# Performance work log

Measured on AMD Instinct MI355X. Metric: run time of the kernel, lower is better.

The kernel has to match this reference:

```python
import jax, jax.numpy as jnp
import numpy as np

# LightGCN propagation constants
N_USERS = 50000
N_ITEMS = 100000
N_NODES = N_USERS + N_ITEMS          # rows of the symmetric normalized adjacency
N_EDGES = 2400000                    # nnz of sparse adjacency (avg degree ~16)
LATENT_DIM = 64                      # config['latent_dim_rec']
N_LAYERS = 3                         # config['lightGCN_n_layers']
BATCH = 4096


def setup_inputs() -> dict:
    key = jax.random.key(0)
    ks = jax.random.split(key, 7)
    # Embedding tables, init std=0.1 as in nn.init.normal_(std=0.1)
    emb_user = 0.1 * jax.random.normal(ks[0], (N_USERS, LATENT_DIM), dtype=jnp.float32)
    emb_item = 0.1 * jax.random.normal(ks[1], (N_ITEMS, LATENT_DIM), dtype=jnp.float32)
    # Sparse normalized adjacency in COO form (fixed structure reused every layer)
    src = jax.random.randint(ks[2], (N_EDGES,), 0, N_NODES, dtype=jnp.int32)
    dst = jax.random.randint(ks[3], (N_EDGES,), 0, N_NODES, dtype=jnp.int32)
    # values ~ 1/sqrt(deg_i * deg_j) scale for avg degree 16
    vals = jax.random.uniform(ks[4], (N_EDGES,), dtype=jnp.float32) / 16.0
    users = jax.random.randint(ks[5], (BATCH,), 0, N_USERS, dtype=jnp.int32)
    items = jax.random.randint(ks[6], (BATCH,), 0, N_ITEMS, dtype=jnp.int32)
    return {"emb_user": emb_user, "emb_item": emb_item, "vals": vals,
            "src": src, "dst": dst, "users": users, "items": items}


def _spmm(vals, src, dst, x):
    # y[dst] += vals * x[src]  == torch.sparse.mm(G, x)
    return jax.ops.segment_sum(vals[:, None] * x[src], dst, num_segments=N_NODES)


def reference(emb_user, emb_item, vals, src, dst, users, items):
    # computer(): stack layer embeddings and mean-pool, fused as running sum
    all_emb = jnp.concatenate([emb_user, emb_item], axis=0)  # [N, D]
    acc = all_emb
    x = all_emb
    for _ in range(N_LAYERS):
        x = _spmm(vals, src, dst, x)
        acc = acc + x
    light_out = acc / jnp.asarray(N_LAYERS + 1, dtype=acc.dtype)
    users_emb = light_out[users]                 # [B, D]
    items_emb = light_out[N_USERS + items]       # [B, D]
    gamma = jnp.sum(users_emb * items_emb, axis=1)  # [B]
    return gamma
```

## Files before the change

kernel.cpp:

```cpp
#include <hip/hip_runtime.h>


#define N_USERS 50000
#define N_ITEMS 100000
#define N_NODES 150000
#define N_EDGES 2400000
#define DIM 64
#define BATCH 4096

#define CHUNKS 512
#define CHUNK_EDGES 4688
#define PPT 5
#define KB 256
#define NPB 586
#define ECAP 10240
#define MAXIT 10
#define GSTR 16
#define NF4 2400000

typedef unsigned int uint;
typedef float v2f __attribute__((ext_vector_type(2)));

__device__ __forceinline__ uint pack_bf16(float a, float b) {
    uint ua = __float_as_uint(a), ub = __float_as_uint(b);
    ua = (ua + 0x7FFFu + ((ua >> 16) & 1u)) >> 16;
    ub = (ub + 0x7FFFu + ((ub >> 16) & 1u)) >> 16;
    return ua | (ub << 16);
}

__device__ __forceinline__ v2f unpack_bf16x2(uint w) {
    v2f r;
    r.x = __uint_as_float(w << 16);
    r.y = __uint_as_float(w & 0xFFFF0000u);
    return r;
}

__global__ __launch_bounds__(1024) void part_kernel(
        const int* __restrict__ src, const int* __restrict__ dstA,
        const float* __restrict__ vals, int* __restrict__ gcur,
        int2* __restrict__ coarse,
        const float* __restrict__ emb_user, const float* __restrict__ emb_item,
        uint2* __restrict__ t0) {
    int t = threadIdx.x;
    __shared__ int2 stage[CHUNK_EDGES];
    __shared__ unsigned char stage_b[CHUNK_EDGES];
    __shared__ int h[KB];
    __shared__ int hoff[KB];
    __shared__ int delta[KB];
    __shared__ int wsum4[4];
    int c = blockIdx.x;
    if (t < KB) h[t] = 0;
    __syncthreads();
    int base = c * CHUNK_EDGES;
    int ecnt = min(CHUNK_EDGES, N_EDGES - base);
    int d_c[PPT];
    int r_c[PPT];
    int s_c[PPT];
    int v_c[PPT];
#pragma unroll
    for (int u = 0; u < PPT; ++u) {
        int i = t + u * 1024;
        d_c[u] = 0;
        r_c[u] = 0;
        s_c[u] = 0;
        v_c[u] = 0;
        if (i < ecnt) {
            int d = dstA[base + i];
            s_c[u] = src[base + i];
            v_c[u] = ((const int*)vals)[base + i];
            d_c[u] = d;
            r_c[u] = atomicAdd(&h[(int)((unsigned)d / NPB)], 1);
        }
    }
    __syncthreads();
    int lane = t & 63, wid = t >> 6;
    if (t < KB) {
        int v = h[t];
        int incl = v;
#pragma unroll
        for (int o = 1; o < 64; o <<= 1) {
            int add = __shfl_up(incl, o, 64);
            if (lane >= o) incl += add;
        }
        hoff[t] = incl - v;
        if (lane == 63) wsum4[wid] = incl;
    }
    __syncthreads();
    if (t < 64) {
        int vv = (lane < 4) ? wsum4[lane] : 0;
        int inc2 = vv;
#pragma unroll
        for (int o = 1; o < 4; o <<= 1) {
            int add = __shfl_up(inc2, o, 64);
            if (lane >= o) inc2 += add;
        }
        if (lane < 4) wsum4[lane] = inc2 - vv;
    }
    __syncthreads();
    if (t < KB) {
        int off = hoff[t] + wsum4[t >> 6];
        hoff[t] = off;
        int cb = atomicAdd(&gcur[t * GSTR], h[t]);
        delta[t] = t * ECAP + cb - off;
    }
    __syncthreads();
#pragma unroll
    for (int u = 0; u < PPT; ++u) {
        int i = t + u * 1024;
        if (i < ecnt) {
            int d = d_c[u];
            int b = (int)((unsigned)d / NPB);
            int dl = d - b * NPB;
            int pos = hoff[b] + r_c[u];
            stage[pos] = make_int2(s_c[u] | (dl << 18), v_c[u]);
            stage_b[pos] = (unsigned char)b;
        }
    }
    __syncthreads();
#pragma unroll
    for (int u = 0; u < PPT; ++u) {
        int j = t + u * 1024;
        if (j < ecnt) {
            int b = stage_b[j];
            int idx = j + delta[b];
            if (idx < (b + 1) * ECAP)
                coarse[idx] = stage[j];
        }
    }
    const int userN4 = N_USERS * DIM / 4;
    int cbase = c * CHUNK_EDGES;
#pragma unroll
    for (int u = 0; u < PPT; ++u) {
        int i = cbase + t + u * 1024;
        if (i < NF4) {
            float4 v;
            if (i < userN4) v = ((const float4*)emb_user)[i];
            else            v = ((const float4*)emb_item)[i - userN4];
            t0[i] = make_uint2(pack_bf16(v.x, v.y), pack_bf16(v.z, v.w));
        }
    }
}

__global__ __launch_bounds__(1024) void p4f_fine(int2* __restrict__ coarse,
                                                 const int* __restrict__ gcur,
                                                 uint* __restrict__ rowinfo) {
    __shared__ int2 eds[ECAP];
    __shared__ unsigned short iperm[ECAP];
    __shared__ int cnt[640];
    __shared__ int rs_[640];
    __shared__ int wsum[16];
    int k = blockIdx.x, t = threadIdx.x;
    int rbase = k * ECAP;
    int ne = min(gcur[k * GSTR], ECAP);
    for (int i = t; i < ne; i += 1024) eds[i] = coarse[rbase + i];
    if (t < 640) cnt[t] = 0;
    __syncthreads();
    int rr[MAXIT];
#pragma unroll
    for (int u = 0; u < MAXIT; ++u) {
        int i = t + u * 1024;
        rr[u] = 0;
        if (i < ne)
            rr[u] = atomicAdd(&cnt[eds[i].x >> 18], 1);
    }
    __syncthreads();
    int wid = t >> 6, lane = t & 63;
    if (t < 640) {
        int v = cnt[t];
        int incl = v;
#pragma unroll
        for (int o = 1; o < 64; o <<= 1) {
            int add = __shfl_up(incl, o, 64);
            if (lane >= o) incl += add;
        }
        rs_[t] = incl - v;
        if (lane == 63) wsum[wid] = incl;
    }
    __syncthreads();
    if (t < 64) {
        int vv = (lane < 10) ? wsum[lane] : 0;
        int inc2 = vv;
#pragma unroll
        for (int o = 1; o < 16; o <<= 1) {
            int add = __shfl_up(inc2, o, 64);
            if (lane >= o) inc2 += add;
        }
        if (lane < 10) wsum[lane] = inc2 - vv;
    }
    __syncthreads();
    if (t < 640) rs_[t] += wsum[wid];
    __syncthreads();
    int nodes0 = k * NPB;
    int nb = min(NPB, N_NODES - nodes0);
    if (t < nb)
        rowinfo[nodes0 + t] = (uint)(rbase + rs_[t]) | ((uint)cnt[t] << 22);
#pragma unroll
    for (int u = 0; u < MAXIT; ++u) {
        int i = t + u * 1024;
        if (i < ne) {
            int dl = eds[i].x >> 18;
            iperm[rs_[dl] + rr[u]] = (unsigned short)i;
        }
    }
    __syncthreads();
    for (int j = t; j < ne; j += 1024) {
        int2 ev = eds[iperm[j]];
        coarse[rbase + j] = make_int2(ev.x & 0x3FFFF, ev.y);
    }
}

__global__ __launch_bounds__(256) void spmm_kernel(
        const uint* __restrict__ rowinfo, const int2* __restrict__ epair,
        const uint* __restrict__ xin, uint* __restrict__ xout) {
    int wave = (blockIdx.x * 256 + threadIdx.x) >> 6;
    int lane = threadIdx.x & 63;
    int g = lane >> 3;
    int l = lane & 7;
    int n = wave * 8 + g;
    bool live = n < N_NODES;
    uint ri = live ? rowinfo[n] : 0u;
    int s = (int)(ri & 0x3FFFFFu);
    int e = live ? s + (int)(ri >> 22) : s;
    int gbase = g * 8;
    v2f a0 = {0.f, 0.f}, a1 = {0.f, 0.f}, a2 = {0.f, 0.f}, a3 = {0.f, 0.f};
    for (int jb = s; jb < e; jb += 8) {
        int jl = jb + l;
        int2 ev = epair[jl < e ? jl : (e - 1)];
        float vw = (jl < e) ? __int_as_float(ev.y) : 0.f;
        int sx = ev.x;
        int srcs[8];
        float ws[8];
#pragma unroll
        for (int u = 0; u < 8; ++u) {
            srcs[u] = __shfl(sx, gbase + u, 64);
            ws[u]   = __shfl(vw, gbase + u, 64);
        }
        uint4 r[8];
#pragma unroll
        for (int u = 0; u < 8; ++u)
            r[u] = ((const uint4*)(xin + (size_t)srcs[u] * 32))[l];
#pragma unroll
        for (int u = 0; u < 8; ++u) {
            a0 += ws[u] * unpack_bf16x2(r[u].x);
            a1 += ws[u] * unpack_bf16x2(r[u].y);
            a2 += ws[u] * unpack_bf16x2(r[u].z);
            a3 += ws[u] * unpack_bf16x2(r[u].w);
        }
    }
    if (live) {
        uint4 o;
        o.x = pack_bf16(a0.x, a0.y);
        o.y = pack_bf16(a1.x, a1.y);
        o.z = pack_bf16(a2.x, a2.y);
        o.w = pack_bf16(a3.x, a3.y);
        ((uint4*)(xout + (size_t)n * 32))[l] = o;
    }
}

__global__ __launch_bounds__(256) void batch_dot_kernel(
        const int* __restrict__ users, const int* __restrict__ items,
        const float* __restrict__ emb_user, const float* __restrict__ emb_item,
        const uint* __restrict__ x1, const uint* __restrict__ x2,
        const uint* __restrict__ rowinfo, const int2* __restrict__ epair,
        float* __restrict__ out) {
    int b = (blockIdx.x * 256 + threadIdx.x) >> 6;
    int lane = threadIdx.x & 63;
    int hg = (lane >> 4) & 1;
    int l = lane & 15;
    bool isU = lane < 32;
    int idx = isU ? users[b] : items[b];
    int n = isU ? idx : N_USERS + idx;
    uint ri = rowinfo[n];
    int s = (int)(ri & 0x3FFFFFu);
    int e = s + (int)(ri >> 22);
    v2f a0 = {0.f, 0.f}, a1 = {0.f, 0.f};
    for (int j0 = s + hg; j0 < e; j0 += 8) {
        int2 ev[4];
        float vv[4];
        uint2 rr[4];
#pragma unroll
        for (int u = 0; u < 4; ++u) {
            int j = j0 + 2 * u;
            bool p = (u == 0) || (j < e);
            ev[u] = epair[p ? j : j0];
            vv[u] = p ? __int_as_float(ev[u].y) : 0.f;
        }
#pragma unroll
        for (int u = 0; u < 4; ++u)
            rr[u] = ((const uint2*)(x2 + (size_t)ev[u].x * 32))[l];
#pragma unroll
        for (int u = 0; u < 4; ++u) {
            a0 += vv[u] * unpack_bf16x2(rr[u].x);
            a1 += vv[u] * unpack_bf16x2(rr[u].y);
        }
    }
    a0.x += __shfl_xor(a0.x, 16, 64);
    a0.y += __shfl_xor(a0.y, 16, 64);
    a1.x += __shfl_xor(a1.x, 16, 64);
    a1.y += __shfl_xor(a1.y, 16, 64);
    const float* t0row = isU ? (emb_user + (size_t)idx * DIM)
                             : (emb_item + (size_t)idx * DIM);
    float4 x0 = ((const float4*)t0row)[l];
    uint2 w1 = ((const uint2*)(x1 + (size_t)n * 32))[l];
    uint2 w2 = ((const uint2*)(x2 + (size_t)n * 32))[l];
    v2f b10 = unpack_bf16x2(w1.x), b11 = unpack_bf16x2(w1.y);
    v2f b20 = unpack_bf16x2(w2.x), b21 = unpack_bf16x2(w2.y);
    float rx = x0.x + b10.x + b20.x + a0.x;
    float ry = x0.y + b10.y + b20.y + a0.y;
    float rz = x0.z + b11.x + b21.x + a1.x;
    float rw = x0.w + b11.y + b21.y + a1.y;
    float ox = __shfl_xor(rx, 32, 64);
    float oy = __shfl_xor(ry, 32, 64);
    float oz = __shfl_xor(rz, 32, 64);
    float ow = __shfl_xor(rw, 32, 64);
    float p = rx * ox + ry * oy + rz * oz + rw * ow;
#pragma unroll
    for (int o = 1; o < 16; o <<= 1) p += __shfl_xor(p, o, 64);
    if (lane == 0) out[b] = p * (1.0f / 16.0f);
}

extern "C" void kernel_launch(void* const* d_in, const int* in_sizes, int n_in,
                              void* d_out, int out_size, void* d_ws, size_t ws_size,
                              hipStream_t stream) {
    const float* emb_user = (const float*)d_in[0];
    const float* emb_item = (const float*)d_in[1];
    const float* vals     = (const float*)d_in[2];
    const int*   src      = (const int*)d_in[3];
    const int*   dst      = (const int*)d_in[4];
    const int*   users    = (const int*)d_in[5];
    const int*   items    = (const int*)d_in[6];
    float* out = (float*)d_out;

    char* ws = (char*)d_ws;
    size_t off = 0;
    auto walloc = [&](size_t bytes) -> void* {
        void* p = ws + off;
        off += (bytes + 255) & ~(size_t)255;
        return p;
    };
    const size_t ROWB = (size_t)N_NODES * DIM * 2;
    uint* t0          = (uint*)walloc(ROWB);
    uint* x1          = (uint*)walloc(ROWB);
    uint* x2          = (uint*)walloc(ROWB);
    int2* coarse      = (int2*)walloc((size_t)KB * ECAP * 8);
    int*  gcur        = (int*) walloc((size_t)KB * GSTR * 4);
    uint* rowinfo     = (uint*)walloc((size_t)N_NODES * 4);

    hipMemsetAsync(gcur, 0, (size_t)KB * GSTR * 4, stream);

    part_kernel<<<CHUNKS, 1024, 0, stream>>>(
        src, dst, vals, gcur, coarse, emb_user, emb_item, (uint2*)t0);
    p4f_fine<<<KB, 1024, 0, stream>>>(coarse, gcur, rowinfo);

    const int SPMM_BLOCKS = (N_NODES / 8 * 64 + 255) / 256;
    spmm_kernel<<<SPMM_BLOCKS, 256, 0, stream>>>(rowinfo, coarse, t0, x1);
    spmm_kernel<<<SPMM_BLOCKS, 256, 0, stream>>>(rowinfo, coarse, x1, x2);
    batch_dot_kernel<<<(BATCH * 64) / 256, 256, 0, stream>>>(
        users, items, emb_user, emb_item, x1, x2, rowinfo, coarse, out);
}
```

Before: 236.9 us.

## Fuse first SpMM layer into fine partition kernel using shared-memory edges

The fine partitioning kernel now runs the first propagation layer itself. It reads the sorted edges and per-row offsets directly from LDS and writes x1, which removes one spmm launch and the global re-read of the edge list and row info for that layer. The cost is parallelism: the fused layer runs on only 256 large blocks, one per CU given the LDS footprint, instead of many small blocks. Gather latency may therefore be less well hidden, and any tail imbalance between blocks now also holds up the partition work.

```diff
diff --git a/kernel.cpp b/kernel.cpp
--- a/kernel.cpp
+++ b/kernel.cpp
@@ -141,9 +141,10 @@
     }
 }
 
-__global__ __launch_bounds__(1024) void p4f_fine(int2* __restrict__ coarse,
-                                                 const int* __restrict__ gcur,
-                                                 uint* __restrict__ rowinfo) {
+__global__ __launch_bounds__(1024) void p4f_spmm(
+        int2* __restrict__ coarse, const int* __restrict__ gcur,
+        uint* __restrict__ rowinfo,
+        const uint* __restrict__ xin, uint* __restrict__ xout) {
     __shared__ int2 eds[ECAP];
     __shared__ unsigned short iperm[ECAP];
     __shared__ int cnt[640];
@@ -206,6 +207,49 @@
     for (int j = t; j < ne; j += 1024) {
         int2 ev = eds[iperm[j]];
         coarse[rbase + j] = make_int2(ev.x & 0x3FFFF, ev.y);
+    }
+    int wave = t >> 6;
+    int g = lane >> 3;
+    int l = lane & 7;
+    for (int dl0 = 0; dl0 < NPB; dl0 += 128) {
+        int dl = dl0 + wave * 8 + g;
+        bool live = dl < nb;
+        int s = live ? rs_[dl] : 0;
+        int e = live ? s + cnt[dl] : 0;
+        v2f a0 = {0.f, 0.f}, a1 = {0.f, 0.f}, a2 = {0.f, 0.f}, a3 = {0.f, 0.f};
+        for (int jb = s; jb < e; jb += 8) {
+            int idxs[8];
+#pragma unroll
+            for (int u = 0; u < 8; ++u) {
+                int j = jb + u;
+                idxs[u] = iperm[j < e ? j : (e - 1)];
+            }
+            int2 ev[8];
+#pragma unroll
+            for (int u = 0; u < 8; ++u) ev[u] = eds[idxs[u]];
+            uint4 r[8];
+#pragma unroll
+            for (int u = 0; u < 8; ++u)
+                r[u] = ((const uint4*)(xin +
+                          (size_t)(ev[u].x & 0x3FFFF) * 32))[l];
+#pragma unroll
+            for (int u = 0; u < 8; ++u) {
+                int j = jb + u;
+                float vw = (j < e) ? __int_as_float(ev[u].y) : 0.f;
+                a0 += vw * unpack_bf16x2(r[u].x);
+                a1 += vw * unpack_bf16x2(r[u].y);
+                a2 += vw * unpack_bf16x2(r[u].z);
+                a3 += vw * unpack_bf16x2(r[u].w);
+            }
+        }
+        if (live) {
+            uint4 o;
+            o.x = pack_bf16(a0.x, a0.y);
+            o.y = pack_bf16(a1.x, a1.y);
+            o.z = pack_bf16(a2.x, a2.y);
+            o.w = pack_bf16(a3.x, a3.y);
+            ((uint4*)(xout + (size_t)(nodes0 + dl) * 32))[l] = o;
+        }
     }
 }
 
@@ -350,10 +394,9 @@
 
     part_kernel<<<CHUNKS, 1024, 0, stream>>>(
         src, dst, vals, gcur, coarse, emb_user, emb_item, (uint2*)t0);
-    p4f_fine<<<KB, 1024, 0, stream>>>(coarse, gcur, rowinfo);
+    p4f_spmm<<<KB, 1024, 0, stream>>>(coarse, gcur, rowinfo, t0, x1);
 
     const int SPMM_BLOCKS = (N_NODES / 8 * 64 + 255) / 256;
-    spmm_kernel<<<SPMM_BLOCKS, 256, 0, stream>>>(rowinfo, coarse, t0, x1);
     spmm_kernel<<<SPMM_BLOCKS, 256, 0, stream>>>(rowinfo, coarse, x1, x2);
     batch_dot_kernel<<<(BATCH * 64) / 256, 256, 0, stream>>>(
         users, items, emb_user, emb_item, x1, x2, rowinfo, coarse, out);
```

New measurement: 230.3 us. 2.8% less time.
